# Kernel tuning notes

Hardware: AMD Instinct MI355X
Metric: run time of the kernel (lower is better)

Reference implementation:

```python
import jax, jax.numpy as jnp
import numpy as np

D, N, P = 512, 256, 256   # state, control, obs dims
H = 16                    # h (and h_tilde, since __init__ sets h_tilde = h)
M_LEN = 24                # m (and m_tilde, since __init__ sets m_tilde = m)
L = 2048                  # history length


def setup_inputs() -> dict:
    key = jax.random.key(0)
    ks = jax.random.split(key, 12)
    A = jax.random.normal(ks[0], (D, D), jnp.float32)
    A = 0.99 * A / jnp.linalg.norm(A, ord=2)  # stable dynamics: spectral radius < 1
    B = jax.random.normal(ks[1], (D, N), jnp.float32) * 0.1
    C = jax.random.normal(ks[2], (P, D), jnp.float32) * 0.1
    M = jax.random.normal(ks[3], (H + 1, H + 1, N, P), jnp.float32) * 0.05
    M_bar = jax.random.normal(ks[4], (H + 1, N, P), jnp.float32) * 0.05
    sigma = jax.random.uniform(ks[5], (H + 1,), jnp.float32) * 0.9 + 0.1    # positive eigvals
    phi = jax.random.normal(ks[6], (M_LEN + 1, H + 1), jnp.float32) * 0.2
    lambda_e = jax.random.uniform(ks[7], (H,), jnp.float32) * 0.9 + 0.1     # positive eigvals
    phi_tilde = jax.random.normal(ks[8], (M_LEN, H), jnp.float32) * 0.2
    y_history = jax.random.normal(ks[9], (L, P), jnp.float32)
    u_history = jax.random.normal(ks[10], (L, N), jnp.float32) * 0.1
    y_nat_history = jax.random.normal(ks[11], (L, P), jnp.float32)
    return dict(A=A, B=B, C=C, M=M, M_bar=M_bar, sigma=sigma, phi=phi,
                lambda_e=lambda_e, phi_tilde=phi_tilde, y_history=y_history,
                u_history=u_history, y_nat_history=y_nat_history)


def reference(A, B, C, M, M_bar, sigma, phi, lambda_e, phi_tilde,
              y_history, u_history, y_nat_history):
    # ---- compute_natural_observation: y_nat = y_t - C * sum_i A^i B u_{t-i} ----
    # Horner recurrence over time order: s <- A s + B u_j  =>  s = sum_i A^i B u_{t-i}
    def nat_step(s, u):
        return A @ s + B @ u, None
    s, _ = jax.lax.scan(nat_step, jnp.zeros((D,), A.dtype), u_history)
    y_nat = y_history[-1] - C @ s                              # (P,)

    # ---- compute_predicted_state: y_nat + sum_{i<h} C A^i B u_{-(i+1)} ----
    def g_step(Apow, _):
        return Apow @ A, C @ Apow @ B                          # G_i = C A^i B, (P, N)
    _, G = jax.lax.scan(g_step, jnp.eye(D, dtype=A.dtype), None, length=H)
    u_rev = u_history[::-1]                                    # u_rev[i] = u_{-(i+1)}
    pred = y_nat + jnp.einsum('ipn,in->p', G, u_rev[:H])

    # ---- compute_control_new (full branch; L >= m + m_tilde + 1) ----
    Yrev = y_nat_history[::-1]                                 # Yrev[k] = y_nat_{-(k+1)}
    lam4 = lambda_e ** 0.25                                    # (H,)
    sig4 = sigma ** 0.25                                       # (H+1,)
    # term 1: M_bar[0] @ y[-1]
    u_t = M_bar[0] @ Yrev[0]
    # term 2: sum_{i<h_t, j<m_t} lam_i^.25 phi_tilde[j,i] M_bar[i+1] @ y[-(j+2)]
    u_t = u_t + jnp.einsum('i,ji,inp,jp->n', lam4, phi_tilde,
                           M_bar[1:], Yrev[1:1 + M_LEN])
    # term 3: sum_{l<=h, k<=m} sig_l^.25 phi[k,l] M[0,l] @ y[-(k+1)]
    u_t = u_t + jnp.einsum('l,kl,lnp,kp->n', sig4, phi, M[0], Yrev[:M_LEN + 1])
    # term 4: sum_{i,j,l,k} (sig_l lam_i)^.25 phi[k,l] phi_tilde[j,i] M[i+1,l] @ y[-(j+k+2)]
    jk = jnp.arange(M_LEN)[:, None] + jnp.arange(M_LEN + 1)[None, :]  # (m_t, m+1)
    Ylag = Yrev[2:2 + 2 * M_LEN]                               # covers lags j+k+2
    Yjk = Ylag[jk]                                             # (m_t, m+1, P)
    u_t = u_t + jnp.einsum('i,l,kl,ji,jkp,ilnp->n', lam4, sig4, phi,
                           phi_tilde, Yjk, M[1:])
    return jnp.concatenate([y_nat, pred, u_t])                 # (2P + N,)
```

## Files before the change

kernel.cpp:

```cpp
#include <hip/hip_runtime.h>

#define L_HIST 2048
typedef unsigned short ushortT;
typedef __attribute__((ext_vector_type(8))) short bf16x8;
typedef __attribute__((ext_vector_type(4))) short bf16x4;
typedef __attribute__((ext_vector_type(16))) float f32x16;

__device__ __forceinline__ ushortT f2bf(float x) {
  union { float f; unsigned u; } v; v.f = x;
  unsigned r = (v.u + 0x7FFFu + ((v.u >> 16) & 1u)) >> 16;
  return (ushortT)r;
}
__device__ __forceinline__ float bf2f(ushortT h) {
  union { unsigned u; float f; } v; v.u = ((unsigned)h) << 16; return v.f;
}
__device__ __forceinline__ bf16x4 lo4(bf16x8 v) {
  return __builtin_shufflevector(v, v, 0, 1, 2, 3);
}
__device__ __forceinline__ bf16x4 hi4(bf16x8 v) {
  return __builtin_shufflevector(v, v, 4, 5, 6, 7);
}
__device__ __forceinline__ bf16x8 rd8(const ushortT* p) {
  bf16x4 a = *(const bf16x4*)p, b = *(const bf16x4*)(p + 4);
  return __builtin_shufflevector(a, b, 0, 1, 2, 3, 4, 5, 6, 7);
}

struct Job {
  const ushortT *Ph, *Qh, *Ql;
  ushortT *Ch, *Cl;
  float *Cf;
  int M, tbase;
};
struct Prm { Job j[3]; int nj; };

__global__ __launch_bounds__(256) void bgemm(Prm p) {
  int bx = blockIdx.x;
  int ji = 0;
  if (p.nj > 1 && bx >= p.j[1].tbase) ji = 1;
  if (p.nj > 2 && bx >= p.j[2].tbase) ji = 2;
  Job J = p.j[ji];
  int lt = bx - J.tbase;
  int mt = J.M >> 6;
  int mtile = lt % mt, ntile = lt / mt;
  size_t m0 = (size_t)mtile * 64, n0 = (size_t)ntile * 64;

  __shared__ ushortT As[4][64][36];
  __shared__ ushortT Bhs[4][64][36];
  __shared__ ushortT Bls[4][64][36];

  int tid = threadIdx.x;
  int lane = tid & 63, wave = tid >> 6;
  int wm = (wave & 1) * 32, wn = (wave >> 1) * 32;
  int fr = lane & 31, fk = (lane >> 5) * 8;
  int row = tid >> 2, kp = (tid & 3) * 8;

  const ushortT* pA  = J.Ph + (m0 + row) * 512 + kp;
  const ushortT* pBh = J.Qh + (n0 + row) * 512 + kp;
  const ushortT* pBl = J.Ql + (n0 + row) * 512 + kp;

  bf16x8 rA[4], rBh[4], rBl[4];
#pragma unroll
  for (int s = 0; s < 4; ++s) {
    rA[s]  = *(const bf16x8*)(pA  + s * 32);
    rBh[s] = *(const bf16x8*)(pBh + s * 32);
    rBl[s] = *(const bf16x8*)(pBl + s * 32);
  }

  f32x16 acc;
#pragma unroll
  for (int i = 0; i < 16; ++i) acc[i] = 0.f;

  for (int c = 0; c < 4; ++c) {
#pragma unroll
    for (int s = 0; s < 4; ++s) {
      *(bf16x4*)&As[s][row][kp]      = lo4(rA[s]);
      *(bf16x4*)&As[s][row][kp + 4]  = hi4(rA[s]);
      *(bf16x4*)&Bhs[s][row][kp]     = lo4(rBh[s]);
      *(bf16x4*)&Bhs[s][row][kp + 4] = hi4(rBh[s]);
      *(bf16x4*)&Bls[s][row][kp]     = lo4(rBl[s]);
      *(bf16x4*)&Bls[s][row][kp + 4] = hi4(rBl[s]);
    }
    __syncthreads();
    if (c < 3) {
      int off = (c + 1) * 128;
#pragma unroll
      for (int s = 0; s < 4; ++s) {
        rA[s]  = *(const bf16x8*)(pA  + off + s * 32);
        rBh[s] = *(const bf16x8*)(pBh + off + s * 32);
        rBl[s] = *(const bf16x8*)(pBl + off + s * 32);
      }
    }
#pragma unroll
    for (int s = 0; s < 4; ++s)
#pragma unroll
      for (int ks = 0; ks < 32; ks += 16) {
        bf16x8 a  = rd8(&As[s][wm + fr][ks + fk]);
        bf16x8 bh = rd8(&Bhs[s][wn + fr][ks + fk]);
        bf16x8 bl = rd8(&Bls[s][wn + fr][ks + fk]);
        acc = __builtin_amdgcn_mfma_f32_32x32x16_bf16(a, bh, acc, 0, 0, 0);
        acc = __builtin_amdgcn_mfma_f32_32x32x16_bf16(a, bl, acc, 0, 0, 0);
      }
    __syncthreads();
  }
#pragma unroll
  for (int i = 0; i < 16; ++i) {
    int r = wm + (i & 3) + ((i >> 2) << 3) + ((lane >> 5) << 2);
    int c = wn + (lane & 31);
    float v = acc[i];
    size_t off = (m0 + r) * 512 + (n0 + c);
    ushortT h = f2bf(v);
    J.Ch[off] = h;
    if (J.Cl) J.Cl[off] = f2bf(v - bf2f(h));
    if (J.Cf) J.Cf[off] = v;
  }
}

__global__ __launch_bounds__(256) void qgemm(
    const ushortT* __restrict__ WTh, const ushortT* __restrict__ UTh,
    const ushortT* __restrict__ UTl, float* __restrict__ Qpart) {
  int z = blockIdx.x, mtile = blockIdx.y, ntile = blockIdx.z;
  int m0 = mtile * 64, n0 = ntile * 64, k0 = z * 1024;

  __shared__ ushortT As[4][64][36];
  __shared__ ushortT Bhs[4][64][36];
  __shared__ ushortT Bls[4][64][36];

  int tid = threadIdx.x;
  int lane = tid & 63, wave = tid >> 6;
  int wm = (wave & 1) * 32, wn = (wave >> 1) * 32;
  int fr = lane & 31, fk = (lane >> 5) * 8;
  int ka = tid & 31, ma = (tid >> 5) * 8;
  int jb = tid >> 2, kb = (tid & 3) * 8;

  const ushortT* pW  = WTh + (size_t)(k0 + ka) * 512 + m0 + ma;
  const ushortT* pUh = UTh + (size_t)(n0 + jb) * 8192 + k0 + kb;
  const ushortT* pUl = UTl + (size_t)(n0 + jb) * 8192 + k0 + kb;

  bf16x8 rW[4], rUh[4], rUl[4];
#pragma unroll
  for (int s = 0; s < 4; ++s) {
    rW[s]  = *(const bf16x8*)(pW + (size_t)(s * 32) * 512);
    rUh[s] = *(const bf16x8*)(pUh + s * 32);
    rUl[s] = *(const bf16x8*)(pUl + s * 32);
  }

  f32x16 acc;
#pragma unroll
  for (int i = 0; i < 16; ++i) acc[i] = 0.f;

  for (int c = 0; c < 8; ++c) {
#pragma unroll
    for (int s = 0; s < 4; ++s) {
#pragma unroll
      for (int e = 0; e < 8; ++e) As[s][ma + e][ka] = (ushortT)rW[s][e];
      *(bf16x4*)&Bhs[s][jb][kb]     = lo4(rUh[s]);
      *(bf16x4*)&Bhs[s][jb][kb + 4] = hi4(rUh[s]);
      *(bf16x4*)&Bls[s][jb][kb]     = lo4(rUl[s]);
      *(bf16x4*)&Bls[s][jb][kb + 4] = hi4(rUl[s]);
    }
    __syncthreads();
    if (c < 7) {
      int off = (c + 1) * 128;
#pragma unroll
      for (int s = 0; s < 4; ++s) {
        rW[s]  = *(const bf16x8*)(pW + (size_t)(off + s * 32) * 512);
        rUh[s] = *(const bf16x8*)(pUh + off + s * 32);
        rUl[s] = *(const bf16x8*)(pUl + off + s * 32);
      }
    }
#pragma unroll
    for (int s = 0; s < 4; ++s)
#pragma unroll
      for (int ks = 0; ks < 32; ks += 16) {
        bf16x8 a  = rd8(&As[s][wm + fr][ks + fk]);
        bf16x8 bh = rd8(&Bhs[s][wn + fr][ks + fk]);
        bf16x8 bl = rd8(&Bls[s][wn + fr][ks + fk]);
        acc = __builtin_amdgcn_mfma_f32_32x32x16_bf16(a, bh, acc, 0, 0, 0);
        acc = __builtin_amdgcn_mfma_f32_32x32x16_bf16(a, bl, acc, 0, 0, 0);
      }
    __syncthreads();
  }
#pragma unroll
  for (int i = 0; i < 16; ++i) {
    int r = wm + (i & 3) + ((i >> 2) << 3) + ((lane >> 5) << 2);
    int c = wn + (lane & 31);
    Qpart[((size_t)z * 512 + m0 + r) * 128 + n0 + c] = acc[i];
  }
}

__global__ void init_all(const float* __restrict__ A, const float* __restrict__ B,
                         const float* __restrict__ uh,
                         ushortT* N1h, ushortT* N1l, ushortT* T1h, ushortT* T1l,
                         ushortT* WTh, ushortT* UTh, ushortT* UTl) {
  int idx = blockIdx.x * 256 + threadIdx.x;
  if (idx < 262144) {
    int r = idx >> 9, c = idx & 511;
    float x = A[idx];
    ushortT h = f2bf(x); ushortT l = f2bf(x - bf2f(h));
    N1h[idx] = h; N1l[idx] = l;
    T1h[c * 512 + r] = h; T1l[c * 512 + r] = l;
  } else if (idx < 262144 + 131072) {
    int i2 = idx - 262144;
    int d = i2 >> 8, c = i2 & 255;
    WTh[c * 512 + d] = f2bf(B[i2]);
  } else {
    int i2 = idx - 393216;
    int j = i2 >> 13, k = i2 & 8191;
    int tau = k >> 8, c = k & 255;
    float v = 0.f;
    if (j < 64) v = uh[(size_t)(L_HIST - 1 - (32 * j + tau)) * 256 + c];
    else if (j == 64 && tau < 16) v = uh[(size_t)(L_HIST - 1 - tau) * 256 + c];
    ushortT h = f2bf(v);
    UTh[i2] = h; UTl[i2] = f2bf(v - bf2f(h));
  }
}

__global__ __launch_bounds__(512) void rgemm(const float* __restrict__ Pf1,
                                             const float* __restrict__ Qpart,
                                             float* __restrict__ Rpart) {
  int j1 = blockIdx.x + 1;
  int dc = blockIdx.y;
  int d0 = dc * 128;
  int m = threadIdx.x;
  __shared__ float Qs[128][8];
  for (int i = threadIdx.x; i < 1024; i += 512) {
    int dd = i >> 3, jj = i & 7;
    float s = 0.f;
#pragma unroll
    for (int z = 0; z < 8; ++z)
      s += Qpart[((size_t)z * 512 + d0 + dd) * 128 + j1 + 8 * jj];
    Qs[dd][jj] = s;
  }
  __syncthreads();
  float acc[8];
#pragma unroll
  for (int jj = 0; jj < 8; ++jj) acc[jj] = 0.f;
  for (int d = 0; d < 128; ++d) {
    float tv = Pf1[((size_t)(j1 - 1) * 512 + d0 + d) * 512 + m];
    float4 q0 = *(const float4*)&Qs[d][0];
    float4 q1 = *(const float4*)&Qs[d][4];
    acc[0] += tv * q0.x; acc[1] += tv * q0.y; acc[2] += tv * q0.z; acc[3] += tv * q0.w;
    acc[4] += tv * q1.x; acc[5] += tv * q1.y; acc[6] += tv * q1.z; acc[7] += tv * q1.w;
  }
  float* dst = Rpart + (size_t)((j1 - 1) * 4 + dc) * 4096 + m * 8;
#pragma unroll
  for (int jj = 0; jj < 8; ++jj) dst[jj] = acc[jj];
}

__global__ __launch_bounds__(512) void sgemm(const float* __restrict__ Pf2,
                                             const float* __restrict__ Qpart,
                                             const float* __restrict__ Rpart,
                                             float* __restrict__ Spart) {
  int j2 = blockIdx.x + 1;
  int dc = blockIdx.y;
  int d0 = dc * 128;
  int m = threadIdx.x;
  __shared__ float Rs[128];
  if (threadIdx.x < 128) {
    int dd = threadIdx.x;
    float s = 0.f;
#pragma unroll
    for (int z = 0; z < 8; ++z)
      s += Qpart[((size_t)z * 512 + d0 + dd) * 128 + 8 * j2];
    for (int p = 0; p < 28; ++p)
      s += Rpart[(size_t)p * 4096 + (d0 + dd) * 8 + j2];
    Rs[dd] = s;
  }
  __syncthreads();
  float acc = 0.f;
  for (int d = 0; d < 128; ++d)
    acc += Pf2[((size_t)(j2 - 1) * 512 + d0 + d) * 512 + m] * Rs[d];
  Spart[(size_t)((j2 - 1) * 4 + dc) * 512 + m] = acc;
}

__global__ __launch_bounds__(64) void finalize_kernel(
    const float* __restrict__ Cmat, const float* __restrict__ Qpart,
    const float* __restrict__ Rpart, const float* __restrict__ Spart,
    const float* __restrict__ yh, float* __restrict__ out) {
  int p = blockIdx.x;
  int lane = threadIdx.x;
  float a1 = 0.f, a2 = 0.f;
  for (int t = lane; t < 512; t += 64) {
    float sb = 0.f, qp = 0.f;
#pragma unroll
    for (int z = 0; z < 8; ++z) {
      sb += Qpart[((size_t)z * 512 + t) * 128 + 0];
      qp += Qpart[((size_t)z * 512 + t) * 128 + 64];
    }
    for (int q = 0; q < 28; ++q) {
      sb += Rpart[(size_t)q * 4096 + t * 8];
      sb += Spart[(size_t)q * 512 + t];
    }
    float cv = Cmat[(size_t)p * 512 + t];
    a1 += cv * sb;
    a2 += cv * qp;
  }
  for (int off = 32; off > 0; off >>= 1) {
    a1 += __shfl_down(a1, off);
    a2 += __shfl_down(a2, off);
  }
  if (lane == 0) {
    float ynat = yh[(size_t)(L_HIST - 1) * 256 + p] - a1;
    out[p] = ynat;
    out[256 + p] = ynat + a2;
  }
}

__global__ __launch_bounds__(256) void weights_kernel(
    const float* __restrict__ ynh, const float* __restrict__ sigma,
    const float* __restrict__ phi, const float* __restrict__ lambda_e,
    const float* __restrict__ phi_tilde, float* __restrict__ wvec,
    float* __restrict__ out) {
  int v = blockIdx.x;
  int p = threadIdx.x;
  __shared__ float w4[48];
  float val = 0.f;
  if (v == 0) {
    val = ynh[(size_t)(L_HIST - 1) * 256 + p];
    out[512 + p] = 0.f;
  } else if (v <= 16) {
    int i = v - 1;
    float s = 0.f;
    for (int j = 0; j < 24; ++j)
      s += phi_tilde[j * 16 + i] * ynh[(size_t)(L_HIST - 2 - j) * 256 + p];
    val = powf(lambda_e[i], 0.25f) * s;
  } else if (v <= 33) {
    int l = v - 17;
    float s = 0.f;
    for (int k = 0; k < 25; ++k)
      s += phi[k * 17 + l] * ynh[(size_t)(L_HIST - 1 - k) * 256 + p];
    val = powf(sigma[l], 0.25f) * s;
  } else {
    int t = v - 34;
    int i = t / 17, l = t % 17;
    if (p < 48) {
      int m = p;
      int jlo = m - 24; if (jlo < 0) jlo = 0;
      int jhi = m; if (jhi > 23) jhi = 23;
      float s = 0.f;
      for (int j = jlo; j <= jhi; ++j)
        s += phi_tilde[j * 16 + i] * phi[(m - j) * 17 + l];
      w4[p] = s;
    }
    __syncthreads();
    float s = 0.f;
    for (int m = 0; m < 48; ++m)
      s += w4[m] * ynh[(size_t)(L_HIST - 3 - m) * 256 + p];
    val = powf(lambda_e[i], 0.25f) * powf(sigma[l], 0.25f) * s;
  }
  wvec[v * 256 + p] = val;
}

__global__ __launch_bounds__(256) void ut_gemv(
    const float* __restrict__ Mtens, const float* __restrict__ Mbar,
    const float* __restrict__ wvec, float* __restrict__ out) {
  int n = blockIdx.x & 255;
  int h = blockIdx.x >> 8;
  int lane = threadIdx.x & 63;
  int wid = threadIdx.x >> 6;
  int vs = (306 * h) >> 2, ve = (306 * (h + 1)) >> 2;
  float4 acc = {0.f, 0.f, 0.f, 0.f};
#pragma unroll 4
  for (int v = vs + wid; v < ve; v += 4) {
    const float* mat = (v < 17 ? Mbar : Mtens - 17 * 65536) + (size_t)v * 65536;
    float4 mv = ((const float4*)(mat + (size_t)n * 256))[lane];
    float4 wv = ((const float4*)(wvec + (size_t)v * 256))[lane];
    acc.x += mv.x * wv.x; acc.y += mv.y * wv.y;
    acc.z += mv.z * wv.z; acc.w += mv.w * wv.w;
  }
  float a = (acc.x + acc.y) + (acc.z + acc.w);
  for (int off = 32; off > 0; off >>= 1) a += __shfl_down(a, off);
  if (lane == 0) atomicAdd(&out[512 + n], a);
}

extern "C" void kernel_launch(void* const* d_in, const int* in_sizes, int n_in,
                              void* d_out, int out_size, void* d_ws, size_t ws_size,
                              hipStream_t stream) {
  (void)in_sizes; (void)n_in; (void)out_size; (void)ws_size;
  const float* A   = (const float*)d_in[0];
  const float* B   = (const float*)d_in[1];
  const float* C   = (const float*)d_in[2];
  const float* M   = (const float*)d_in[3];
  const float* Mb  = (const float*)d_in[4];
  const float* sig = (const float*)d_in[5];
  const float* phi = (const float*)d_in[6];
  const float* lam = (const float*)d_in[7];
  const float* pt  = (const float*)d_in[8];
  const float* yh  = (const float*)d_in[9];
  const float* uh  = (const float*)d_in[10];
  const float* ynh = (const float*)d_in[11];
  float* out = (float*)d_out;
  char* base = (char*)d_ws;

  const size_t MB = 1u << 20;
  const size_t SL = 512 * 512;
  ushortT* POW  = (ushortT*)base;
  ushortT* WTh  = (ushortT*)(base + 16 * MB);
  ushortT* P1th = (ushortT*)(base + 26 * MB);
  ushortT* P1tl = (ushortT*)(base + 30 * MB);
  ushortT* P2th = (ushortT*)(base + 34 * MB);
  ushortT* P2tl = (ushortT*)(base + 38 * MB);
  float*   Pf1  = (float*)(base + 42 * MB);
  float*   Pf2  = (float*)(base + 50 * MB);
  ushortT* UTh  = (ushortT*)(base + 58 * MB);
  ushortT* UTl  = (ushortT*)(base + 60 * MB);
  float*   Qpart= (float*)(base + 62 * MB);
  float*   Rpart= (float*)(base + 64 * MB);
  float*   Spart= Rpart + 28 * 4096;
  float*   wvec = Spart + 28 * 512;

  auto ph = [&](int i) { return POW + (size_t)i * 2 * SL; };
  auto pl = [&](int i) { return POW + (size_t)i * 2 * SL + SL; };
  auto e1h = [&](int j) { return P1th + (size_t)(j - 1) * SL; };
  auto e1l = [&](int j) { return P1tl + (size_t)(j - 1) * SL; };
  auto e2h = [&](int j) { return P2th + (size_t)(j - 1) * SL; };
  auto e2l = [&](int j) { return P2tl + (size_t)(j - 1) * SL; };

  auto mkJ = [&](const ushortT* Ph, const ushortT* Qh, const ushortT* Ql,
                 ushortT* Ch, ushortT* Cl, float* Cf, int Mrows) {
    Job j; j.Ph = Ph; j.Qh = Qh; j.Ql = Ql;
    j.Ch = Ch; j.Cl = Cl; j.Cf = Cf; j.M = Mrows; j.tbase = 0; return j;
  };
  auto runL = [&](Job j0, Job j1, Job j2, int nj) {
    Prm p; p.j[0] = j0; p.j[1] = (nj > 1) ? j1 : j0; p.j[2] = (nj > 2) ? j2 : j0;
    p.nj = nj;
    int tb = 0;
    for (int i = 0; i < nj; ++i) { p.j[i].tbase = tb; tb += (p.j[i].M >> 6) * 8; }
    bgemm<<<tb, 256, 0, stream>>>(p);
  };

  init_all<<<5632, 256, 0, stream>>>(A, B, uh, ph(0), pl(0), ph(1), pl(1),
                                     WTh, UTh, UTl);

  Job d = mkJ(ph(0), ph(1), pl(1), ph(2), pl(2), nullptr, 512);
  runL(mkJ(ph(0), ph(1), pl(1), ph(2), pl(2), nullptr, 512),
       mkJ(ph(1), ph(0), pl(0), ph(3), pl(3), nullptr, 512),
       mkJ(WTh, ph(0), pl(0), WTh + 256 * 512, nullptr, nullptr, 256), 3);
  runL(mkJ(ph(2), ph(3), pl(3), ph(4), pl(4), nullptr, 512),
       mkJ(ph(3), ph(2), pl(2), ph(5), pl(5), nullptr, 512),
       mkJ(WTh, ph(2), pl(2), WTh + 512 * 512, nullptr, nullptr, 512), 3);
  runL(mkJ(ph(4), ph(5), pl(5), ph(6), pl(6), nullptr, 512),
       mkJ(ph(5), ph(4), pl(4), ph(7), pl(7), nullptr, 512),
       mkJ(WTh, ph(4), pl(4), WTh + 1024 * 512, nullptr, nullptr, 1024), 3);
  runL(mkJ(ph(6), ph(7), pl(7), ph(8), pl(8), nullptr, 512),
       mkJ(ph(7), ph(6), pl(6), ph(9), pl(9), nullptr, 512),
       mkJ(WTh, ph(6), pl(6), WTh + 2048 * 512, nullptr, nullptr, 2048), 3);
  runL(mkJ(ph(8), ph(9), pl(9), ph(10), pl(10), nullptr, 512),
       mkJ(ph(9), ph(8), pl(8), e1h(1), e1l(1), Pf1, 512),
       mkJ(WTh, ph(8), pl(8), WTh + 4096 * 512, nullptr, nullptr, 4096), 3);
  runL(mkJ(ph(10), e1h(1), e1l(1), ph(11), pl(11), nullptr, 512),
       mkJ(e1h(1), ph(10), pl(10), e1h(2), e1l(2), Pf1 + SL, 512),
       d, 2);
  runL(mkJ(ph(11), e1h(2), e1l(2), ph(12), pl(12), nullptr, 512),
       mkJ(e1h(1), ph(11), pl(11), e1h(3), e1l(3), Pf1 + 2 * SL, 1024),
       d, 2);
  runL(mkJ(ph(12), e1h(4), e1l(4), ph(13), pl(13), nullptr, 512),
       mkJ(e1h(1), ph(12), pl(12), e1h(5), nullptr, Pf1 + 4 * SL, 1536),
       mkJ(e1h(4), ph(12), pl(12), e2h(1), e2l(1), Pf2, 512), 3);
  runL(mkJ(ph(13), e2h(1), e2l(1), ph(14), pl(14), nullptr, 512),
       mkJ(e2h(1), ph(13), pl(13), e2h(2), e2l(2), Pf2 + SL, 512),
       d, 2);
  runL(mkJ(ph(14), e2h(2), e2l(2), ph(15), pl(15), nullptr, 512),
       mkJ(e2h(1), ph(14), pl(14), e2h(3), nullptr, Pf2 + 2 * SL, 1024),
       d, 2);
  runL(mkJ(e2h(1), ph(15), pl(15), e2h(5), nullptr, Pf2 + 4 * SL, 1536),
       d, d, 1);

  qgemm<<<dim3(8, 8, 2), 256, 0, stream>>>(WTh, UTh, UTl, Qpart);
  rgemm<<<dim3(7, 4), 512, 0, stream>>>(Pf1, Qpart, Rpart);
  sgemm<<<dim3(7, 4), 512, 0, stream>>>(Pf2, Qpart, Rpart, Spart);
  finalize_kernel<<<256, 64, 0, stream>>>(C, Qpart, Rpart, Spart, yh, out);

  weights_kernel<<<306, 256, 0, stream>>>(ynh, sig, phi, lam, pt, wvec, out);
  ut_gemv<<<1024, 256, 0, stream>>>(M, Mb, wvec, out);
}
```

Baseline: 310.7 us.

## Merge independent qgemm, rgemm and u_t gemv work into bgemm launches

Turns the batched GEMM kernel into a mega-kernel whose extra blocks also run the Q GEMM (split 16 ways over K instead of 8), the R reduction GEMM, and slices of the u_t GEMV. These blocks are spread across the power-squaring launches so they fill idle CUs. The weights computation moves into the init kernel, and the workspace layout is compacted. This removes several launches and the serial tail at the cost of more complex dispatch and more partial sums to reduce.

```diff
diff --git a/kernel.cpp b/kernel.cpp
--- a/kernel.cpp
+++ b/kernel.cpp
@@ -31,10 +31,139 @@
   float *Cf;
   int M, tbase;
 };
-struct Prm { Job j[3]; int nj; };
-
-__global__ __launch_bounds__(256) void bgemm(Prm p) {
+struct Prm {
+  Job j[3]; int nj;
+  int qbase, rbase, utbase, uv0;
+  const ushortT *Wt, *Uh, *Ul;
+  float *Qp;
+  const float *Pf1; float *Rp;
+  const float *Mt, *Mbar, *wv; float *outp;
+};
+
+__global__ __launch_bounds__(256) void mega(Prm p) {
+  __shared__ __align__(16) ushortT As[4][64][36];
+  __shared__ ushortT Bhs[4][64][36];
+  __shared__ ushortT Bls[4][64][36];
   int bx = blockIdx.x;
+  int tid = threadIdx.x;
+
+  if (bx >= p.utbase) {
+    int u = bx - p.utbase + p.uv0;
+    int n = u & 255, h = u >> 8;
+    int lane = tid & 63, wid = tid >> 6;
+    int vs = (306 * h) >> 2, ve = (306 * (h + 1)) >> 2;
+    float4 acc = {0.f, 0.f, 0.f, 0.f};
+#pragma unroll 4
+    for (int v = vs + wid; v < ve; v += 4) {
+      const float* mat = (v < 17 ? p.Mbar : p.Mt - 17 * 65536) + (size_t)v * 65536;
+      float4 mv = ((const float4*)(mat + (size_t)n * 256))[lane];
+      float4 wv = ((const float4*)(p.wv + (size_t)v * 256))[lane];
+      acc.x += mv.x * wv.x; acc.y += mv.y * wv.y;
+      acc.z += mv.z * wv.z; acc.w += mv.w * wv.w;
+    }
+    float a = (acc.x + acc.y) + (acc.z + acc.w);
+    for (int off = 32; off > 0; off >>= 1) a += __shfl_down(a, off);
+    if (lane == 0) atomicAdd(&p.outp[512 + n], a);
+    return;
+  }
+
+  if (bx >= p.rbase) {
+    int r = bx - p.rbase;
+    float* Qs = (float*)&As[0][0][0];
+    int pr = r >> 1, mh = r & 1;
+    int j1 = (pr >> 2) + 1, dc = pr & 3;
+    int d0 = dc * 128, m = mh * 256 + tid;
+    for (int i = tid; i < 1024; i += 256) {
+      int dd = i >> 3, jj = i & 7;
+      float s = 0.f;
+#pragma unroll
+      for (int z = 0; z < 16; ++z)
+        s += p.Qp[((size_t)z * 512 + d0 + dd) * 128 + j1 + 8 * jj];
+      Qs[dd * 8 + jj] = s;
+    }
+    __syncthreads();
+    float acc[8];
+#pragma unroll
+    for (int jj = 0; jj < 8; ++jj) acc[jj] = 0.f;
+    for (int d = 0; d < 128; ++d) {
+      float tv = p.Pf1[((size_t)(j1 - 1) * 512 + d0 + d) * 512 + m];
+      float4 q0 = *(const float4*)&Qs[d * 8];
+      float4 q1 = *(const float4*)&Qs[d * 8 + 4];
+      acc[0] += tv * q0.x; acc[1] += tv * q0.y; acc[2] += tv * q0.z; acc[3] += tv * q0.w;
+      acc[4] += tv * q1.x; acc[5] += tv * q1.y; acc[6] += tv * q1.z; acc[7] += tv * q1.w;
+    }
+    float* dst = p.Rp + (size_t)((j1 - 1) * 4 + dc) * 4096 + m * 8;
+#pragma unroll
+    for (int jj = 0; jj < 8; ++jj) dst[jj] = acc[jj];
+    return;
+  }
+
+  if (bx >= p.qbase) {
+    int q = bx - p.qbase;
+    int z = q & 15, mtile = (q >> 4) & 7, ntile = q >> 7;
+    int m0 = mtile * 64, n0 = ntile * 64, k0 = z * 512;
+    int lane = tid & 63, wave = tid >> 6;
+    int wm = (wave & 1) * 32, wn = (wave >> 1) * 32;
+    int fr = lane & 31, fk = (lane >> 5) * 8;
+    int ka = tid & 31, ma = (tid >> 5) * 8;
+    int jb = tid >> 2, kb = (tid & 3) * 8;
+
+    const ushortT* pW  = p.Wt + (size_t)(k0 + ka) * 512 + m0 + ma;
+    const ushortT* pUh = p.Uh + (size_t)(n0 + jb) * 8192 + k0 + kb;
+    const ushortT* pUl = p.Ul + (size_t)(n0 + jb) * 8192 + k0 + kb;
+
+    bf16x8 rW[4], rUh[4], rUl[4];
+#pragma unroll
+    for (int s = 0; s < 4; ++s) {
+      rW[s]  = *(const bf16x8*)(pW + (size_t)(s * 32) * 512);
+      rUh[s] = *(const bf16x8*)(pUh + s * 32);
+      rUl[s] = *(const bf16x8*)(pUl + s * 32);
+    }
+    f32x16 acc;
+#pragma unroll
+    for (int i = 0; i < 16; ++i) acc[i] = 0.f;
+
+    for (int c = 0; c < 4; ++c) {
+#pragma unroll
+      for (int s = 0; s < 4; ++s) {
+#pragma unroll
+        for (int e = 0; e < 8; ++e) As[s][ma + e][ka] = (ushortT)rW[s][e];
+        *(bf16x4*)&Bhs[s][jb][kb]     = lo4(rUh[s]);
+        *(bf16x4*)&Bhs[s][jb][kb + 4] = hi4(rUh[s]);
+        *(bf16x4*)&Bls[s][jb][kb]     = lo4(rUl[s]);
+        *(bf16x4*)&Bls[s][jb][kb + 4] = hi4(rUl[s]);
+      }
+      __syncthreads();
+      if (c < 3) {
+        int off = (c + 1) * 128;
+#pragma unroll
+        for (int s = 0; s < 4; ++s) {
+          rW[s]  = *(const bf16x8*)(pW + (size_t)(off + s * 32) * 512);
+          rUh[s] = *(const bf16x8*)(pUh + off + s * 32);
+          rUl[s] = *(const bf16x8*)(pUl + off + s * 32);
+        }
+      }
+#pragma unroll
+      for (int s = 0; s < 4; ++s)
+#pragma unroll
+        for (int ks = 0; ks < 32; ks += 16) {
+          bf16x8 a  = rd8(&As[s][wm + fr][ks + fk]);
+          bf16x8 bh = rd8(&Bhs[s][wn + fr][ks + fk]);
+          bf16x8 bl = rd8(&Bls[s][wn + fr][ks + fk]);
+          acc = __builtin_amdgcn_mfma_f32_32x32x16_bf16(a, bh, acc, 0, 0, 0);
+          acc = __builtin_amdgcn_mfma_f32_32x32x16_bf16(a, bl, acc, 0, 0, 0);
+        }
+      __syncthreads();
+    }
+#pragma unroll
+    for (int i = 0; i < 16; ++i) {
+      int rr = wm + (i & 3) + ((i >> 2) << 3) + ((lane >> 5) << 2);
+      int cc = wn + (lane & 31);
+      p.Qp[((size_t)z * 512 + m0 + rr) * 128 + n0 + cc] = acc[i];
+    }
+    return;
+  }
+
   int ji = 0;
   if (p.nj > 1 && bx >= p.j[1].tbase) ji = 1;
   if (p.nj > 2 && bx >= p.j[2].tbase) ji = 2;
@@ -44,11 +173,6 @@
   int mtile = lt % mt, ntile = lt / mt;
   size_t m0 = (size_t)mtile * 64, n0 = (size_t)ntile * 64;
 
-  __shared__ ushortT As[4][64][36];
-  __shared__ ushortT Bhs[4][64][36];
-  __shared__ ushortT Bls[4][64][36];
-
-  int tid = threadIdx.x;
   int lane = tid & 63, wave = tid >> 6;
   int wm = (wave & 1) * 32, wn = (wave >> 1) * 32;
   int fr = lane & 31, fk = (lane >> 5) * 8;
@@ -115,83 +239,56 @@
   }
 }
 
-__global__ __launch_bounds__(256) void qgemm(
-    const ushortT* __restrict__ WTh, const ushortT* __restrict__ UTh,
-    const ushortT* __restrict__ UTl, float* __restrict__ Qpart) {
-  int z = blockIdx.x, mtile = blockIdx.y, ntile = blockIdx.z;
-  int m0 = mtile * 64, n0 = ntile * 64, k0 = z * 1024;
-
-  __shared__ ushortT As[4][64][36];
-  __shared__ ushortT Bhs[4][64][36];
-  __shared__ ushortT Bls[4][64][36];
-
-  int tid = threadIdx.x;
-  int lane = tid & 63, wave = tid >> 6;
-  int wm = (wave & 1) * 32, wn = (wave >> 1) * 32;
-  int fr = lane & 31, fk = (lane >> 5) * 8;
-  int ka = tid & 31, ma = (tid >> 5) * 8;
-  int jb = tid >> 2, kb = (tid & 3) * 8;
-
-  const ushortT* pW  = WTh + (size_t)(k0 + ka) * 512 + m0 + ma;
-  const ushortT* pUh = UTh + (size_t)(n0 + jb) * 8192 + k0 + kb;
-  const ushortT* pUl = UTl + (size_t)(n0 + jb) * 8192 + k0 + kb;
-
-  bf16x8 rW[4], rUh[4], rUl[4];
-#pragma unroll
-  for (int s = 0; s < 4; ++s) {
-    rW[s]  = *(const bf16x8*)(pW + (size_t)(s * 32) * 512);
-    rUh[s] = *(const bf16x8*)(pUh + s * 32);
-    rUl[s] = *(const bf16x8*)(pUl + s * 32);
-  }
-
-  f32x16 acc;
-#pragma unroll
-  for (int i = 0; i < 16; ++i) acc[i] = 0.f;
-
-  for (int c = 0; c < 8; ++c) {
-#pragma unroll
-    for (int s = 0; s < 4; ++s) {
-#pragma unroll
-      for (int e = 0; e < 8; ++e) As[s][ma + e][ka] = (ushortT)rW[s][e];
-      *(bf16x4*)&Bhs[s][jb][kb]     = lo4(rUh[s]);
-      *(bf16x4*)&Bhs[s][jb][kb + 4] = hi4(rUh[s]);
-      *(bf16x4*)&Bls[s][jb][kb]     = lo4(rUl[s]);
-      *(bf16x4*)&Bls[s][jb][kb + 4] = hi4(rUl[s]);
-    }
-    __syncthreads();
-    if (c < 7) {
-      int off = (c + 1) * 128;
-#pragma unroll
-      for (int s = 0; s < 4; ++s) {
-        rW[s]  = *(const bf16x8*)(pW + (size_t)(off + s * 32) * 512);
-        rUh[s] = *(const bf16x8*)(pUh + off + s * 32);
-        rUl[s] = *(const bf16x8*)(pUl + off + s * 32);
+__global__ __launch_bounds__(256) void init_all(
+    const float* __restrict__ A, const float* __restrict__ B,
+    const float* __restrict__ uh,
+    ushortT* N1h, ushortT* N1l, ushortT* T1h, ushortT* T1l,
+    ushortT* WTh, ushortT* UTh, ushortT* UTl,
+    const float* __restrict__ ynh, const float* __restrict__ sigma,
+    const float* __restrict__ phi, const float* __restrict__ lambda_e,
+    const float* __restrict__ phi_tilde, float* __restrict__ wvec,
+    float* __restrict__ out) {
+  __shared__ float w4[48];
+  if (blockIdx.x >= 5632) {
+    int v = blockIdx.x - 5632;
+    int p = threadIdx.x;
+    float val = 0.f;
+    if (v == 0) {
+      val = ynh[(size_t)(L_HIST - 1) * 256 + p];
+      out[512 + p] = 0.f;
+    } else if (v <= 16) {
+      int i = v - 1;
+      float s = 0.f;
+      for (int j = 0; j < 24; ++j)
+        s += phi_tilde[j * 16 + i] * ynh[(size_t)(L_HIST - 2 - j) * 256 + p];
+      val = powf(lambda_e[i], 0.25f) * s;
+    } else if (v <= 33) {
+      int l = v - 17;
+      float s = 0.f;
+      for (int k = 0; k < 25; ++k)
+        s += phi[k * 17 + l] * ynh[(size_t)(L_HIST - 1 - k) * 256 + p];
+      val = powf(sigma[l], 0.25f) * s;
+    } else {
+      int t = v - 34;
+      int i = t / 17, l = t % 17;
+      if (p < 48) {
+        int m = p;
+        int jlo = m - 24; if (jlo < 0) jlo = 0;
+        int jhi = m; if (jhi > 23) jhi = 23;
+        float s = 0.f;
+        for (int j = jlo; j <= jhi; ++j)
+          s += phi_tilde[j * 16 + i] * phi[(m - j) * 17 + l];
+        w4[p] = s;
       }
-    }
-#pragma unroll
-    for (int s = 0; s < 4; ++s)
-#pragma unroll
-      for (int ks = 0; ks < 32; ks += 16) {
-        bf16x8 a  = rd8(&As[s][wm + fr][ks + fk]);
-        bf16x8 bh = rd8(&Bhs[s][wn + fr][ks + fk]);
-        bf16x8 bl = rd8(&Bls[s][wn + fr][ks + fk]);
-        acc = __builtin_amdgcn_mfma_f32_32x32x16_bf16(a, bh, acc, 0, 0, 0);
-        acc = __builtin_amdgcn_mfma_f32_32x32x16_bf16(a, bl, acc, 0, 0, 0);
-      }
-    __syncthreads();
-  }
-#pragma unroll
-  for (int i = 0; i < 16; ++i) {
-    int r = wm + (i & 3) + ((i >> 2) << 3) + ((lane >> 5) << 2);
-    int c = wn + (lane & 31);
-    Qpart[((size_t)z * 512 + m0 + r) * 128 + n0 + c] = acc[i];
-  }
-}
-
-__global__ void init_all(const float* __restrict__ A, const float* __restrict__ B,
-                         const float* __restrict__ uh,
-                         ushortT* N1h, ushortT* N1l, ushortT* T1h, ushortT* T1l,
-                         ushortT* WTh, ushortT* UTh, ushortT* UTl) {
+      __syncthreads();
+      float s = 0.f;
+      for (int m = 0; m < 48; ++m)
+        s += w4[m] * ynh[(size_t)(L_HIST - 3 - m) * 256 + p];
+      val = powf(lambda_e[i], 0.25f) * powf(sigma[l], 0.25f) * s;
+    }
+    wvec[v * 256 + p] = val;
+    return;
+  }
   int idx = blockIdx.x * 256 + threadIdx.x;
   if (idx < 262144) {
     int r = idx >> 9, c = idx & 511;
@@ -215,38 +312,6 @@
   }
 }
 
-__global__ __launch_bounds__(512) void rgemm(const float* __restrict__ Pf1,
-                                             const float* __restrict__ Qpart,
-                                             float* __restrict__ Rpart) {
-  int j1 = blockIdx.x + 1;
-  int dc = blockIdx.y;
-  int d0 = dc * 128;
-  int m = threadIdx.x;
-  __shared__ float Qs[128][8];
-  for (int i = threadIdx.x; i < 1024; i += 512) {
-    int dd = i >> 3, jj = i & 7;
-    float s = 0.f;
-#pragma unroll
-    for (int z = 0; z < 8; ++z)
-      s += Qpart[((size_t)z * 512 + d0 + dd) * 128 + j1 + 8 * jj];
-    Qs[dd][jj] = s;
-  }
-  __syncthreads();
-  float acc[8];
-#pragma unroll
-  for (int jj = 0; jj < 8; ++jj) acc[jj] = 0.f;
-  for (int d = 0; d < 128; ++d) {
-    float tv = Pf1[((size_t)(j1 - 1) * 512 + d0 + d) * 512 + m];
-    float4 q0 = *(const float4*)&Qs[d][0];
-    float4 q1 = *(const float4*)&Qs[d][4];
-    acc[0] += tv * q0.x; acc[1] += tv * q0.y; acc[2] += tv * q0.z; acc[3] += tv * q0.w;
-    acc[4] += tv * q1.x; acc[5] += tv * q1.y; acc[6] += tv * q1.z; acc[7] += tv * q1.w;
-  }
-  float* dst = Rpart + (size_t)((j1 - 1) * 4 + dc) * 4096 + m * 8;
-#pragma unroll
-  for (int jj = 0; jj < 8; ++jj) dst[jj] = acc[jj];
-}
-
 __global__ __launch_bounds__(512) void sgemm(const float* __restrict__ Pf2,
                                              const float* __restrict__ Qpart,
                                              const float* __restrict__ Rpart,
@@ -260,7 +325,7 @@
     int dd = threadIdx.x;
     float s = 0.f;
 #pragma unroll
-    for (int z = 0; z < 8; ++z)
+    for (int z = 0; z < 16; ++z)
       s += Qpart[((size_t)z * 512 + d0 + dd) * 128 + 8 * j2];
     for (int p = 0; p < 28; ++p)
       s += Rpart[(size_t)p * 4096 + (d0 + dd) * 8 + j2];
@@ -283,7 +348,7 @@
   for (int t = lane; t < 512; t += 64) {
     float sb = 0.f, qp = 0.f;
 #pragma unroll
-    for (int z = 0; z < 8; ++z) {
+    for (int z = 0; z < 16; ++z) {
       sb += Qpart[((size_t)z * 512 + t) * 128 + 0];
       qp += Qpart[((size_t)z * 512 + t) * 128 + 64];
     }
@@ -304,73 +369,6 @@
     out[p] = ynat;
     out[256 + p] = ynat + a2;
   }
-}
-
-__global__ __launch_bounds__(256) void weights_kernel(
-    const float* __restrict__ ynh, const float* __restrict__ sigma,
-    const float* __restrict__ phi, const float* __restrict__ lambda_e,
-    const float* __restrict__ phi_tilde, float* __restrict__ wvec,
-    float* __restrict__ out) {
-  int v = blockIdx.x;
-  int p = threadIdx.x;
-  __shared__ float w4[48];
-  float val = 0.f;
-  if (v == 0) {
-    val = ynh[(size_t)(L_HIST - 1) * 256 + p];
-    out[512 + p] = 0.f;
-  } else if (v <= 16) {
-    int i = v - 1;
-    float s = 0.f;
-    for (int j = 0; j < 24; ++j)
-      s += phi_tilde[j * 16 + i] * ynh[(size_t)(L_HIST - 2 - j) * 256 + p];
-    val = powf(lambda_e[i], 0.25f) * s;
-  } else if (v <= 33) {
-    int l = v - 17;
-    float s = 0.f;
-    for (int k = 0; k < 25; ++k)
-      s += phi[k * 17 + l] * ynh[(size_t)(L_HIST - 1 - k) * 256 + p];
-    val = powf(sigma[l], 0.25f) * s;
-  } else {
-    int t = v - 34;
-    int i = t / 17, l = t % 17;
-    if (p < 48) {
-      int m = p;
-      int jlo = m - 24; if (jlo < 0) jlo = 0;
-      int jhi = m; if (jhi > 23) jhi = 23;
-      float s = 0.f;
-      for (int j = jlo; j <= jhi; ++j)
-        s += phi_tilde[j * 16 + i] * phi[(m - j) * 17 + l];
-      w4[p] = s;
-    }
-    __syncthreads();
-    float s = 0.f;
-    for (int m = 0; m < 48; ++m)
-      s += w4[m] * ynh[(size_t)(L_HIST - 3 - m) * 256 + p];
-    val = powf(lambda_e[i], 0.25f) * powf(sigma[l], 0.25f) * s;
-  }
-  wvec[v * 256 + p] = val;
-}
-
-__global__ __launch_bounds__(256) void ut_gemv(
-    const float* __restrict__ Mtens, const float* __restrict__ Mbar,
-    const float* __restrict__ wvec, float* __restrict__ out) {
-  int n = blockIdx.x & 255;
-  int h = blockIdx.x >> 8;
-  int lane = threadIdx.x & 63;
-  int wid = threadIdx.x >> 6;
-  int vs = (306 * h) >> 2, ve = (306 * (h + 1)) >> 2;
-  float4 acc = {0.f, 0.f, 0.f, 0.f};
-#pragma unroll 4
-  for (int v = vs + wid; v < ve; v += 4) {
-    const float* mat = (v < 17 ? Mbar : Mtens - 17 * 65536) + (size_t)v * 65536;
-    float4 mv = ((const float4*)(mat + (size_t)n * 256))[lane];
-    float4 wv = ((const float4*)(wvec + (size_t)v * 256))[lane];
-    acc.x += mv.x * wv.x; acc.y += mv.y * wv.y;
-    acc.z += mv.z * wv.z; acc.w += mv.w * wv.w;
-  }
-  float a = (acc.x + acc.y) + (acc.z + acc.w);
-  for (int off = 32; off > 0; off >>= 1) a += __shfl_down(a, off);
-  if (lane == 0) atomicAdd(&out[512 + n], a);
 }
 
 extern "C" void kernel_launch(void* const* d_in, const int* in_sizes, int n_in,
@@ -392,20 +390,20 @@
   float* out = (float*)d_out;
   char* base = (char*)d_ws;
 
-  const size_t MB = 1u << 20;
+  const size_t HMB = 512u * 1024u;
   const size_t SL = 512 * 512;
   ushortT* POW  = (ushortT*)base;
-  ushortT* WTh  = (ushortT*)(base + 16 * MB);
-  ushortT* P1th = (ushortT*)(base + 26 * MB);
-  ushortT* P1tl = (ushortT*)(base + 30 * MB);
-  ushortT* P2th = (ushortT*)(base + 34 * MB);
-  ushortT* P2tl = (ushortT*)(base + 38 * MB);
-  float*   Pf1  = (float*)(base + 42 * MB);
-  float*   Pf2  = (float*)(base + 50 * MB);
-  ushortT* UTh  = (ushortT*)(base + 58 * MB);
-  ushortT* UTl  = (ushortT*)(base + 60 * MB);
-  float*   Qpart= (float*)(base + 62 * MB);
-  float*   Rpart= (float*)(base + 64 * MB);
+  ushortT* WTh  = (ushortT*)(base + 32 * HMB);
+  ushortT* P1th = (ushortT*)(base + 48 * HMB);
+  ushortT* P1tl = (ushortT*)(base + 55 * HMB);
+  ushortT* P2th = (ushortT*)(base + 62 * HMB);
+  ushortT* P2tl = (ushortT*)(base + 69 * HMB);
+  float*   Pf1  = (float*)(base + 76 * HMB);
+  float*   Pf2  = (float*)(base + 90 * HMB);
+  ushortT* UTh  = (ushortT*)(base + 104 * HMB);
+  ushortT* UTl  = (ushortT*)(base + 108 * HMB);
+  float*   Qpart= (float*)(base + 112 * HMB);
+  float*   Rpart= (float*)(base + 120 * HMB);
   float*   Spart= Rpart + 28 * 4096;
   float*   wvec = Spart + 28 * 512;
 
@@ -421,56 +419,64 @@
     Job j; j.Ph = Ph; j.Qh = Qh; j.Ql = Ql;
     j.Ch = Ch; j.Cl = Cl; j.Cf = Cf; j.M = Mrows; j.tbase = 0; return j;
   };
-  auto runL = [&](Job j0, Job j1, Job j2, int nj) {
+  int uvoff = 0;
+  auto runL = [&](Job j0, Job j1, Job j2, int nj, int qcnt, int rcnt, int utcnt) {
     Prm p; p.j[0] = j0; p.j[1] = (nj > 1) ? j1 : j0; p.j[2] = (nj > 2) ? j2 : j0;
     p.nj = nj;
     int tb = 0;
     for (int i = 0; i < nj; ++i) { p.j[i].tbase = tb; tb += (p.j[i].M >> 6) * 8; }
-    bgemm<<<tb, 256, 0, stream>>>(p);
+    p.qbase = tb; p.rbase = tb + qcnt; p.utbase = p.rbase + rcnt;
+    p.uv0 = uvoff; uvoff += utcnt;
+    p.Wt = WTh; p.Uh = UTh; p.Ul = UTl; p.Qp = Qpart;
+    p.Pf1 = Pf1; p.Rp = Rpart;
+    p.Mt = M; p.Mbar = Mb; p.wv = wvec; p.outp = out;
+    mega<<<p.utbase + utcnt, 256, 0, stream>>>(p);
   };
 
-  init_all<<<5632, 256, 0, stream>>>(A, B, uh, ph(0), pl(0), ph(1), pl(1),
-                                     WTh, UTh, UTl);
+  init_all<<<5938, 256, 0, stream>>>(A, B, uh, ph(0), pl(0), ph(1), pl(1),
+                                     WTh, UTh, UTl,
+                                     ynh, sig, phi, lam, pt, wvec, out);
 
   Job d = mkJ(ph(0), ph(1), pl(1), ph(2), pl(2), nullptr, 512);
   runL(mkJ(ph(0), ph(1), pl(1), ph(2), pl(2), nullptr, 512),
        mkJ(ph(1), ph(0), pl(0), ph(3), pl(3), nullptr, 512),
-       mkJ(WTh, ph(0), pl(0), WTh + 256 * 512, nullptr, nullptr, 256), 3);
+       mkJ(WTh, ph(0), pl(0), WTh + 256 * 512, nullptr, nullptr, 256),
+       3, 0, 0, 93);
   runL(mkJ(ph(2), ph(3), pl(3), ph(4), pl(4), nullptr, 512),
        mkJ(ph(3), ph(2), pl(2), ph(5), pl(5), nullptr, 512),
-       mkJ(WTh, ph(2), pl(2), WTh + 512 * 512, nullptr, nullptr, 512), 3);
+       mkJ(WTh, ph(2), pl(2), WTh + 512 * 512, nullptr, nullptr, 512),
+       3, 0, 0, 93);
   runL(mkJ(ph(4), ph(5), pl(5), ph(6), pl(6), nullptr, 512),
        mkJ(ph(5), ph(4), pl(4), ph(7), pl(7), nullptr, 512),
-       mkJ(WTh, ph(4), pl(4), WTh + 1024 * 512, nullptr, nullptr, 1024), 3);
+       mkJ(WTh, ph(4), pl(4), WTh + 1024 * 512, nullptr, nullptr, 1024),
+       3, 0, 0, 93);
   runL(mkJ(ph(6), ph(7), pl(7), ph(8), pl(8), nullptr, 512),
        mkJ(ph(7), ph(6), pl(6), ph(9), pl(9), nullptr, 512),
-       mkJ(WTh, ph(6), pl(6), WTh + 2048 * 512, nullptr, nullptr, 2048), 3);
+       mkJ(WTh, ph(6), pl(6), WTh + 2048 * 512, nullptr, nullptr, 2048),
+       3, 0, 0, 93);
   runL(mkJ(ph(8), ph(9), pl(9), ph(10), pl(10), nullptr, 512),
        mkJ(ph(9), ph(8), pl(8), e1h(1), e1l(1), Pf1, 512),
-       mkJ(WTh, ph(8), pl(8), WTh + 4096 * 512, nullptr, nullptr, 4096), 3);
+       mkJ(WTh, ph(8), pl(8), WTh + 4096 * 512, nullptr, nullptr, 4096),
+       3, 0, 0, 93);
   runL(mkJ(ph(10), e1h(1), e1l(1), ph(11), pl(11), nullptr, 512),
        mkJ(e1h(1), ph(10), pl(10), e1h(2), e1l(2), Pf1 + SL, 512),
-       d, 2);
+       d, 2, 256, 0, 93);
   runL(mkJ(ph(11), e1h(2), e1l(2), ph(12), pl(12), nullptr, 512),
        mkJ(e1h(1), ph(11), pl(11), e1h(3), e1l(3), Pf1 + 2 * SL, 1024),
-       d, 2);
+       d, 2, 0, 0, 93);
   runL(mkJ(ph(12), e1h(4), e1l(4), ph(13), pl(13), nullptr, 512),
        mkJ(e1h(1), ph(12), pl(12), e1h(5), nullptr, Pf1 + 4 * SL, 1536),
-       mkJ(e1h(4), ph(12), pl(12), e2h(1), e2l(1), Pf2, 512), 3);
+       mkJ(e1h(4), ph(12), pl(12), e2h(1), e2l(1), Pf2, 512),
+       3, 0, 0, 93);
   runL(mkJ(ph(13), e2h(1), e2l(1), ph(14), pl(14), nullptr, 512),
        mkJ(e2h(1), ph(13), pl(13), e2h(2), e2l(2), Pf2 + SL, 512),
-       d, 2);
+       d, 2, 0, 56, 93);
   runL(mkJ(ph(14), e2h(2), e2l(2), ph(15), pl(15), nullptr, 512),
        mkJ(e2h(1), ph(14), pl(14), e2h(3), nullptr, Pf2 + 2 * SL, 1024),
-       d, 2);
+       d, 2, 0, 0, 93);
   runL(mkJ(e2h(1), ph(15), pl(15), e2h(5), nullptr, Pf2 + 4 * SL, 1536),
-       d, d, 1);
-
-  qgemm<<<dim3(8, 8, 2), 256, 0, stream>>>(WTh, UTh, UTl, Qpart);
-  rgemm<<<dim3(7, 4), 512, 0, stream>>>(Pf1, Qpart, Rpart);
+       d, d, 1, 0, 0, 94);
+
   sgemm<<<dim3(7, 4), 512, 0, stream>>>(Pf2, Qpart, Rpart, Spart);
   finalize_kernel<<<256, 64, 0, stream>>>(C, Qpart, Rpart, Spart, yh, out);
-
-  weights_kernel<<<306, 256, 0, stream>>>(ynh, sig, phi, lam, pt, wvec, out);
-  ut_gemv<<<1024, 256, 0, stream>>>(M, Mb, wvec, out);
-}
+}
```

Measured after the change: 299.4 us. -3.6%, faster.
